# Kernel optimization log

Measured on AMD Instinct MI355X. Metric: run time of the kernel, lower is better.

The kernel has to match this reference:

```python
import jax, jax.numpy as jnp
import numpy as np

K_SEM = 5          # max_semantic_edges
THRESH = 0.2       # semantic_threshold
NEG_INF = -1e30


def setup_inputs() -> dict:
    key = jax.random.key(0)
    k1, k2 = jax.random.split(key)
    message_embeddings = jax.random.normal(k1, (8192, 256), dtype=jnp.float32)
    edge_emb_table = jax.random.normal(k2, (2, 64), dtype=jnp.float32)
    return {"message_embeddings": message_embeddings, "edge_emb_table": edge_emb_table}


def reference(message_embeddings, edge_emb_table):
    N = message_embeddings.shape[0]

    # ---- temporal edges: for each i -> [i,i+1] then [i+1,i] (interleaved) ----
    i = jnp.arange(N - 1)
    fwd = jnp.stack([i, i + 1])            # [2, N-1]
    bwd = jnp.stack([i + 1, i])            # [2, N-1]
    temporal = jnp.stack([fwd, bwd], axis=2).reshape(2, -1)   # [2, 2(N-1)]
    n_temporal = 2 * (N - 1)

    # ---- semantic edges: per-row top-k over sim[i, :i] with threshold ----
    norm = jnp.sqrt(jnp.sum(message_embeddings * message_embeddings, axis=1, keepdims=True))
    emb_n = message_embeddings / jnp.maximum(norm, 1e-12)     # F.normalize(p=2)
    sim = emb_n @ emb_n.T                                      # [N, N]

    r = jnp.arange(N)[:, None]
    c = jnp.arange(N)[None, :]
    # zero out diagonal and adjacent (temporal) pairs, as the torch mask does
    sim = sim * (jnp.abs(r - c) > 1)
    # restrict candidates to j < i (strictly earlier messages)
    cand = jnp.where(c < r, sim, NEG_INF)                      # [N, N]

    vals, idxs = jax.lax.top_k(cand, K_SEM)                    # [N, K]
    sem_src = idxs.reshape(-1)                                 # [N*K]
    sem_dst = jnp.repeat(jnp.arange(N), K_SEM)                 # [N*K]
    sem_valid = (vals > THRESH).reshape(-1)                    # [N*K]

    # ---- assemble padded fixed-size edge set ----
    edge_index = jnp.concatenate([temporal, jnp.stack([sem_src, sem_dst])], axis=1)
    edge_types = jnp.concatenate(
        [jnp.zeros((n_temporal,), jnp.int32), jnp.ones((N * K_SEM,), jnp.int32)])
    valid = jnp.concatenate([jnp.ones((n_temporal,), bool), sem_valid])

    edge_attr = edge_emb_table[edge_types] * valid[:, None].astype(edge_emb_table.dtype)
    edge_index = jnp.where(valid[None, :], edge_index, -1)
    return edge_index, edge_attr, valid
```

## Files before the change

### kernel.cpp

```cpp
#include <hip/hip_runtime.h>

#define N_MSG 8192
#define DIM 256
#define KS 5
#define THRESH 0.2f
#define FILT 0.196f
#define N_TEMPORAL (2*(N_MSG-1))
#define N_EDGES (N_TEMPORAL + N_MSG*KS)
#define ATTR_OFF (2*N_EDGES)
#define VALID_OFF (ATTR_OFF + N_EDGES*64)
#define BM 128
#define BN 128
#define NTILE (N_MSG / BM)
#define NBLOCKS (NTILE*(NTILE+1)/2)
#define CAP 32

typedef __bf16 bf16x8 __attribute__((ext_vector_type(8)));
typedef __bf16 bf16x4 __attribute__((ext_vector_type(4)));
typedef float  f32x4  __attribute__((ext_vector_type(4)));

__device__ __forceinline__ void gload_lds16(const void* g, void* l) {
    __builtin_amdgcn_global_load_lds(
        (const __attribute__((address_space(1))) void*)g,
        (__attribute__((address_space(3))) void*)l, 16, 0, 0);
}

__device__ __forceinline__ void ins5(float v, int j, float (&vv)[KS], int (&xx)[KS]) {
    float cv = v; int cj = j;
#pragma unroll
    for (int k = 0; k < KS; ++k) {
        bool b = (cv > vv[k]) || (cv == vv[k] && cj < xx[k]);
        float tv = b ? vv[k] : cv; int tj = b ? xx[k] : cj;
        vv[k] = b ? cv : vv[k];    xx[k] = b ? cj : xx[k];
        cv = tv; cj = tj;
    }
}

__global__ void normalize_k(const float* __restrict__ emb, float* __restrict__ embn,
                            __bf16* __restrict__ embh, int* __restrict__ cnt) {
    int lane = threadIdx.x & 63;
    int row = blockIdx.x * 4 + (threadIdx.x >> 6);
    const float4 x = *(const float4*)(emb + (size_t)row * DIM + lane * 4);
    float ss = x.x * x.x;
    ss = fmaf(x.y, x.y, ss); ss = fmaf(x.z, x.z, ss); ss = fmaf(x.w, x.w, ss);
#pragma unroll
    for (int off = 1; off <= 32; off <<= 1) ss += __shfl_xor(ss, off);
    float nrm = fmaxf(sqrtf(ss), 1e-12f);
    float4 y; y.x = x.x / nrm; y.y = x.y / nrm; y.z = x.z / nrm; y.w = x.w / nrm;
    *(float4*)(embn + (size_t)row * DIM + lane * 4) = y;
    bf16x4 h; h[0] = (__bf16)y.x; h[1] = (__bf16)y.y; h[2] = (__bf16)y.z; h[3] = (__bf16)y.w;
    *(bf16x4*)(embh + (size_t)row * DIM + lane * 4) = h;
    if (lane == 0) cnt[row] = 0;
}

__global__ __launch_bounds__(256, 4)
void sim_filter_k(const __bf16* __restrict__ embh, int* __restrict__ cnt,
                  int* __restrict__ cidx) {
    __shared__ __align__(16) __bf16 As[BM * 32];
    __shared__ __align__(16) __bf16 Bs[BN * 32];

    int t = blockIdx.x;
    int bi = (int)((sqrtf(8.0f * (float)t + 1.0f) - 1.0f) * 0.5f);
    while ((bi + 1) * (bi + 2) / 2 <= t) ++bi;
    while (bi * (bi + 1) / 2 > t) --bi;
    int bj = t - bi * (bi + 1) / 2;
    const int i0 = bi * BM, j0 = bj * BN;

    const int tid = threadIdx.x;
    const int lane = tid & 63;
    const int ws = tid >> 6;
    const int wm = ws >> 1, wn = ws & 1;
    const int lr = lane & 15, kb = lane >> 4;

    const int gm1 = tid & 127, gk1 = tid >> 7;
    const int gm2 = tid & 127, gk2 = (tid >> 7) + 2;

    f32x4 acc[4][4];
#pragma unroll
    for (int m = 0; m < 4; ++m)
#pragma unroll
        for (int n = 0; n < 4; ++n) { f32x4 z = {0.f, 0.f, 0.f, 0.f}; acc[m][n] = z; }

    for (int kt = 0; kt < DIM; kt += 32) {
        __syncthreads();
        gload_lds16(embh + (size_t)(i0 + gm1) * DIM + kt + gk1 * 8, &As[(size_t)tid * 8]);
        gload_lds16(embh + (size_t)(i0 + gm2) * DIM + kt + gk2 * 8, &As[((size_t)tid + 256) * 8]);
        gload_lds16(embh + (size_t)(j0 + gm1) * DIM + kt + gk1 * 8, &Bs[(size_t)tid * 8]);
        gload_lds16(embh + (size_t)(j0 + gm2) * DIM + kt + gk2 * 8, &Bs[((size_t)tid + 256) * 8]);
        __syncthreads();

        bf16x8 a[4], b[4];
#pragma unroll
        for (int f = 0; f < 4; ++f) {
            a[f] = *(const bf16x8*)&As[(kb * 128 + wm * 64 + f * 16 + lr) * 8];
            b[f] = *(const bf16x8*)&Bs[(kb * 128 + wn * 64 + f * 16 + lr) * 8];
        }
#pragma unroll
        for (int m = 0; m < 4; ++m)
#pragma unroll
            for (int n = 0; n < 4; ++n)
                acc[m][n] = __builtin_amdgcn_mfma_f32_16x16x32_bf16(a[m], b[n], acc[m][n], 0, 0, 0);
    }

#pragma unroll
    for (int m = 0; m < 4; ++m) {
        int i = i0 + wm * 64 + m * 16 + kb * 4;
#pragma unroll
        for (int n = 0; n < 4; ++n) {
            int j = j0 + wn * 64 + n * 16 + lr;
#pragma unroll
            for (int r = 0; r < 4; ++r) {
                float v = acc[m][n][r];
                int ii = i + r;
                if (v > FILT && j <= ii - 2) {
                    int c = atomicAdd(&cnt[ii], 1);
                    if (c < CAP) cidx[(size_t)ii * CAP + c] = j;
                }
            }
        }
    }
}

__global__ void rescue_k(const float* __restrict__ embn, const int* __restrict__ cnt,
                         const int* __restrict__ cidx, float* __restrict__ out) {
    int i = blockIdx.x;
    int lane = threadIdx.x;
    int nc = cnt[i]; if (nc > CAP) nc = CAP;

    float fv[KS]; int fx[KS];
#pragma unroll
    for (int k = 0; k < KS; ++k) { fv[k] = -1e30f; fx[k] = -1; }

    if (nc > 0) {
        const float4 a = *(const float4*)(embn + (size_t)i * DIM + lane * 4);
        for (int c = 0; c < nc; ++c) {
            int j = cidx[(size_t)i * CAP + c];
            const float4 b = *(const float4*)(embn + (size_t)j * DIM + lane * 4);
            float p = a.x * b.x;
            p = fmaf(a.y, b.y, p); p = fmaf(a.z, b.z, p); p = fmaf(a.w, b.w, p);
#pragma unroll
            for (int off = 1; off <= 32; off <<= 1) p += __shfl_xor(p, off);
            if (p > THRESH) ins5(p, j, fv, fx);
        }
    }
    int vcnt = 0;
#pragma unroll
    for (int k = 0; k < KS; ++k) vcnt += (fv[k] > THRESH) ? 1 : 0;
    if (lane < KS) {
        int e = N_TEMPORAL + i * KS + lane;
        bool val = (lane < vcnt);
        out[e]             = val ? (float)fx[lane] : -1.0f;
        out[N_EDGES + e]   = val ? (float)i        : -1.0f;
        out[VALID_OFF + e] = val ? 1.0f : 0.0f;
    }
}

__global__ void attr_out_k(const float* __restrict__ table, float* __restrict__ out) {
    int idx = blockIdx.x * 256 + threadIdx.x;
    int e = idx >> 4, sub = idx & 15;
    if (e >= N_EDGES) return;
    float4 a4;
    if (e < N_TEMPORAL) {
        a4 = *(const float4*)(table + sub * 4);
        if (sub == 0) {
            int i = e >> 1;
            out[e]             = (e & 1) ? (float)(i + 1) : (float)i;
            out[N_EDGES + e]   = (e & 1) ? (float)i       : (float)(i + 1);
            out[VALID_OFF + e] = 1.0f;
        }
    } else {
        float vld = out[VALID_OFF + e];
        a4 = *(const float4*)(table + 64 + sub * 4);
        a4.x *= vld; a4.y *= vld; a4.z *= vld; a4.w *= vld;
    }
    *(float4*)(out + ATTR_OFF + (size_t)e * 64 + sub * 4) = a4;
}

extern "C" void kernel_launch(void* const* d_in, const int* in_sizes, int n_in,
                              void* d_out, int out_size, void* d_ws, size_t ws_size,
                              hipStream_t stream) {
    const float* emb   = (const float*)d_in[0];
    const float* table = (const float*)d_in[1];
    float* out = (float*)d_out;

    size_t embn_f  = (size_t)N_MSG * DIM;
    size_t embh_f  = (size_t)N_MSG * DIM / 2;
    size_t cidx_f  = (size_t)N_MSG * CAP;
    size_t cnt_f   = N_MSG;
    size_t need_bytes = (embn_f + embh_f + cidx_f + cnt_f) * 4;

    float* scratch;
    if (ws_size >= need_bytes) scratch = (float*)d_ws;
    else scratch = out + ATTR_OFF;
    float*  embn = scratch;
    __bf16* embh = (__bf16*)(scratch + embn_f);
    int*    cidx = (int*)(scratch + embn_f + embh_f);
    int*    cnt  = (int*)(scratch + embn_f + embh_f + cidx_f);

    normalize_k<<<N_MSG / 4, 256, 0, stream>>>(emb, embn, embh, cnt);
    sim_filter_k<<<NBLOCKS, 256, 0, stream>>>(embh, cnt, cidx);
    rescue_k<<<N_MSG, 64, 0, stream>>>(embn, cnt, cidx, out);
    attr_out_k<<<((size_t)N_EDGES * 16 + 255) / 256, 256, 0, stream>>>(table, out);
}
```

Baseline: 77.50 us.

## Load half-K tiles with XOR swizzle and fuse edge-attr output into rescue kernel

The similarity GEMM now loads 128-wide K slices into swizzled LDS, so it needs two syncs instead of sixteen. The swizzle is meant to avoid LDS bank conflicts. The rescue kernel packs four rows per 256-thread block and, when a workspace is available, also writes the temporal and semantic edge attributes and indices, which removes the separate attr_out pass and its re-read of the valid flags. The trade-off is larger LDS use (64KB), which lowers occupancy (launch bounds drop from 4 to 2), and more per-row writes inside the rescue kernel.

```diff
diff --git a/kernel.cpp b/kernel.cpp
--- a/kernel.cpp
+++ b/kernel.cpp
@@ -10,7 +10,6 @@
 #define ATTR_OFF (2*N_EDGES)
 #define VALID_OFF (ATTR_OFF + N_EDGES*64)
 #define BM 128
-#define BN 128
 #define NTILE (N_MSG / BM)
 #define NBLOCKS (NTILE*(NTILE+1)/2)
 #define CAP 32
@@ -53,18 +52,18 @@
     if (lane == 0) cnt[row] = 0;
 }
 
-__global__ __launch_bounds__(256, 4)
+__global__ __launch_bounds__(256, 2)
 void sim_filter_k(const __bf16* __restrict__ embh, int* __restrict__ cnt,
                   int* __restrict__ cidx) {
-    __shared__ __align__(16) __bf16 As[BM * 32];
-    __shared__ __align__(16) __bf16 Bs[BN * 32];
+    __shared__ __align__(16) __bf16 As[BM * 128];
+    __shared__ __align__(16) __bf16 Bs[BM * 128];
 
     int t = blockIdx.x;
     int bi = (int)((sqrtf(8.0f * (float)t + 1.0f) - 1.0f) * 0.5f);
     while ((bi + 1) * (bi + 2) / 2 <= t) ++bi;
     while (bi * (bi + 1) / 2 > t) --bi;
     int bj = t - bi * (bi + 1) / 2;
-    const int i0 = bi * BM, j0 = bj * BN;
+    const int i0 = bi * BM, j0 = bj * BM;
 
     const int tid = threadIdx.x;
     const int lane = tid & 63;
@@ -72,34 +71,41 @@
     const int wm = ws >> 1, wn = ws & 1;
     const int lr = lane & 15, kb = lane >> 4;
 
-    const int gm1 = tid & 127, gk1 = tid >> 7;
-    const int gm2 = tid & 127, gk2 = (tid >> 7) + 2;
-
     f32x4 acc[4][4];
 #pragma unroll
     for (int m = 0; m < 4; ++m)
 #pragma unroll
         for (int n = 0; n < 4; ++n) { f32x4 z = {0.f, 0.f, 0.f, 0.f}; acc[m][n] = z; }
 
-    for (int kt = 0; kt < DIM; kt += 32) {
+#pragma unroll
+    for (int h = 0; h < 2; ++h) {
+        if (h) __syncthreads();
+#pragma unroll
+        for (int q = 0; q < 8; ++q) {
+            int g = q * 256 + tid;
+            int row = g >> 4, s = g & 15;
+            int sc = s ^ (row & 7);
+            gload_lds16(embh + (size_t)(i0 + row) * DIM + h * 128 + sc * 8, &As[(size_t)g * 8]);
+            gload_lds16(embh + (size_t)(j0 + row) * DIM + h * 128 + sc * 8, &Bs[(size_t)g * 8]);
+        }
         __syncthreads();
-        gload_lds16(embh + (size_t)(i0 + gm1) * DIM + kt + gk1 * 8, &As[(size_t)tid * 8]);
-        gload_lds16(embh + (size_t)(i0 + gm2) * DIM + kt + gk2 * 8, &As[((size_t)tid + 256) * 8]);
-        gload_lds16(embh + (size_t)(j0 + gm1) * DIM + kt + gk1 * 8, &Bs[(size_t)tid * 8]);
-        gload_lds16(embh + (size_t)(j0 + gm2) * DIM + kt + gk2 * 8, &Bs[((size_t)tid + 256) * 8]);
-        __syncthreads();
-
-        bf16x8 a[4], b[4];
-#pragma unroll
-        for (int f = 0; f < 4; ++f) {
-            a[f] = *(const bf16x8*)&As[(kb * 128 + wm * 64 + f * 16 + lr) * 8];
-            b[f] = *(const bf16x8*)&Bs[(kb * 128 + wn * 64 + f * 16 + lr) * 8];
-        }
-#pragma unroll
-        for (int m = 0; m < 4; ++m)
-#pragma unroll
-            for (int n = 0; n < 4; ++n)
-                acc[m][n] = __builtin_amdgcn_mfma_f32_16x16x32_bf16(a[m], b[n], acc[m][n], 0, 0, 0);
+
+#pragma unroll
+        for (int ks = 0; ks < 4; ++ks) {
+            bf16x8 a[4], b[4];
+#pragma unroll
+            for (int f = 0; f < 4; ++f) {
+                int ra = wm * 64 + f * 16 + lr;
+                a[f] = *(const bf16x8*)&As[(size_t)ra * 128 + (((ks * 4 + kb) ^ (ra & 7)) << 3)];
+                int rb = wn * 64 + f * 16 + lr;
+                b[f] = *(const bf16x8*)&Bs[(size_t)rb * 128 + (((ks * 4 + kb) ^ (rb & 7)) << 3)];
+            }
+#pragma unroll
+            for (int m = 0; m < 4; ++m)
+#pragma unroll
+                for (int n = 0; n < 4; ++n)
+                    acc[m][n] = __builtin_amdgcn_mfma_f32_16x16x32_bf16(a[m], b[n], acc[m][n], 0, 0, 0);
+        }
     }
 
 #pragma unroll
@@ -121,10 +127,12 @@
     }
 }
 
+template<bool FUSE>
 __global__ void rescue_k(const float* __restrict__ embn, const int* __restrict__ cnt,
-                         const int* __restrict__ cidx, float* __restrict__ out) {
-    int i = blockIdx.x;
-    int lane = threadIdx.x;
+                         const int* __restrict__ cidx, const float* __restrict__ table,
+                         float* __restrict__ out) {
+    int lane = threadIdx.x & 63;
+    int i = blockIdx.x * 4 + (threadIdx.x >> 6);
     int nc = cnt[i]; if (nc > CAP) nc = CAP;
 
     float fv[KS]; int fx[KS];
@@ -146,12 +154,34 @@
     int vcnt = 0;
 #pragma unroll
     for (int k = 0; k < KS; ++k) vcnt += (fv[k] > THRESH) ? 1 : 0;
-    if (lane < KS) {
-        int e = N_TEMPORAL + i * KS + lane;
-        bool val = (lane < vcnt);
-        out[e]             = val ? (float)fx[lane] : -1.0f;
-        out[N_EDGES + e]   = val ? (float)i        : -1.0f;
-        out[VALID_OFF + e] = val ? 1.0f : 0.0f;
+
+    float tsem = FUSE ? table[64 + lane] : 0.0f;
+#pragma unroll
+    for (int k = 0; k < KS; ++k) {
+        int e = N_TEMPORAL + i * KS + k;
+        bool val = (k < vcnt);
+        if (lane == 0) {
+            out[e]             = val ? (float)fx[k] : -1.0f;
+            out[N_EDGES + e]   = val ? (float)i     : -1.0f;
+            out[VALID_OFF + e] = val ? 1.0f : 0.0f;
+        }
+        if (FUSE) out[ATTR_OFF + (size_t)e * 64 + lane] = val ? tsem : 0.0f;
+    }
+    if (FUSE) {
+        if (i < N_MSG - 1) {
+            float ttem = table[lane];
+            int e0 = 2 * i;
+            out[ATTR_OFF + (size_t)e0 * 64 + lane]       = ttem;
+            out[ATTR_OFF + (size_t)(e0 + 1) * 64 + lane] = ttem;
+            if (lane == 0) {
+                out[e0]                 = (float)i;
+                out[N_EDGES + e0]       = (float)(i + 1);
+                out[VALID_OFF + e0]     = 1.0f;
+                out[e0 + 1]             = (float)(i + 1);
+                out[N_EDGES + e0 + 1]   = (float)i;
+                out[VALID_OFF + e0 + 1] = 1.0f;
+            }
+        }
     }
 }
 
@@ -189,9 +219,9 @@
     size_t cnt_f   = N_MSG;
     size_t need_bytes = (embn_f + embh_f + cidx_f + cnt_f) * 4;
 
-    float* scratch;
-    if (ws_size >= need_bytes) scratch = (float*)d_ws;
-    else scratch = out + ATTR_OFF;
+    bool have_ws = (ws_size >= need_bytes);
+    float* scratch = have_ws ? (float*)d_ws
+                             : out + ATTR_OFF;
     float*  embn = scratch;
     __bf16* embh = (__bf16*)(scratch + embn_f);
     int*    cidx = (int*)(scratch + embn_f + embh_f);
@@ -199,6 +229,10 @@
 
     normalize_k<<<N_MSG / 4, 256, 0, stream>>>(emb, embn, embh, cnt);
     sim_filter_k<<<NBLOCKS, 256, 0, stream>>>(embh, cnt, cidx);
-    rescue_k<<<N_MSG, 64, 0, stream>>>(embn, cnt, cidx, out);
-    attr_out_k<<<((size_t)N_EDGES * 16 + 255) / 256, 256, 0, stream>>>(table, out);
-}
+    if (have_ws) {
+        rescue_k<true><<<N_MSG / 4, 256, 0, stream>>>(embn, cnt, cidx, table, out);
+    } else {
+        rescue_k<false><<<N_MSG / 4, 256, 0, stream>>>(embn, cnt, cidx, table, out);
+        attr_out_k<<<((size_t)N_EDGES * 16 + 255) / 256, 256, 0, stream>>>(table, out);
+    }
+}
```

Result: faster. 67.01 us (-13.5%).
